# Kernel tuning notes

Measured on AMD Instinct MI355X. Metric: run time of the kernel, lower is better.

Reference implementation:

```python
import jax, jax.numpy as jnp
import numpy as np

B, C_IN, L = 16, 64, 1024
HID, OUT, ORDER = 1024, 512, 4
EPS = 1e-5


def setup_inputs() -> dict:
    key = jax.random.key(0)
    ks = jax.random.split(key, 4)
    return {
        "x": jax.random.normal(ks[0], (B, C_IN, L), jnp.float32),
        "W_in": jax.random.normal(ks[1], (C_IN, HID), jnp.float32) / np.sqrt(C_IN).astype(np.float32),
        "b_in": jnp.zeros((HID,), jnp.float32),
        "coeffs1": jax.random.normal(ks[2], (HID, HID, ORDER), jnp.float32) * 0.01,
        "bias1": jnp.zeros((HID,), jnp.float32),
        "g1": jnp.ones((HID,), jnp.float32),
        "beta1": jnp.zeros((HID,), jnp.float32),
        "coeffs2": jax.random.normal(ks[3], (OUT, HID, ORDER), jnp.float32) * 0.01,
        "bias2": jnp.zeros((OUT,), jnp.float32),
        "g2": jnp.ones((OUT,), jnp.float32),
        "beta2": jnp.zeros((OUT,), jnp.float32),
    }


def _taylor_kan(x, coeffs, bias):
    # x: (B, L, C_in); coeffs: (out, C_in, order); y[b,l,o] = sum_i sum_c x^i * coeffs[o,c,i]
    # Expressed as order-wise GEMMs with a running power -- no (B,out,L,C) expand.
    order = coeffs.shape[-1]
    y = jnp.zeros(x.shape[:2] + (coeffs.shape[0],), x.dtype)
    xp = jnp.ones_like(x)  # x**0 (matches torch 0**0 == 1)
    for i in range(order):
        y = y + jnp.einsum('blc,oc->blo', xp, coeffs[:, :, i])
        if i + 1 < order:
            xp = xp * x
    return y + bias


def _layernorm(x, g, b):
    mu = jnp.mean(x, -1, keepdims=True)
    var = jnp.mean((x - mu) ** 2, -1, keepdims=True)
    return (x - mu) * jax.lax.rsqrt(var + EPS) * g + b


def reference(x, W_in, b_in, coeffs1, bias1, g1, beta1, coeffs2, bias2, g2, beta2):
    # x: (B, C_in, L) -> project channels to hidden: (B, L, HID)
    h = jnp.einsum('bcl,ch->blh', x, W_in) + b_in
    h = _taylor_kan(h, coeffs1, bias1)            # (B, L, HID)
    h = jax.nn.gelu(_layernorm(h, g1, beta1), approximate=False)
    h = _taylor_kan(h, coeffs2, bias2)            # (B, L, OUT)
    h = _layernorm(h, g2, beta2)
    return jnp.mean(h, axis=1)                    # adaptive avg pool over L -> (B, OUT)
```

## Files before the change

### kernel.cpp

```cpp
#include <hip/hip_runtime.h>
#include <hip/hip_bf16.h>
#include <math.h>

#define Bsz  16
#define CIN  64
#define LEN  1024
#define HIDN 1024
#define OUTN 512
#define MTOT (Bsz*LEN)
#define KTOT (3*HIDN)
#define KT1  (2*HIDN + CIN)
#define LCHUNKS 32
#define LROWS   (LEN/LCHUNKS)

typedef __attribute__((ext_vector_type(8))) short bf16x8;
typedef __attribute__((ext_vector_type(16))) float f32x16;

__device__ __forceinline__ unsigned short f2bf(float x) {
    union { float f; unsigned int u; } v; v.f = x;
    unsigned int r = v.u + 0x7fff + ((v.u >> 16) & 1);
    return (unsigned short)(r >> 16);
}
__device__ __forceinline__ float bf2f(unsigned short u) {
    union { unsigned int u; float f; } v; v.u = ((unsigned int)u) << 16;
    return v.f;
}
__device__ __forceinline__ void gload_lds16(const void* g, void* l) {
    __builtin_amdgcn_global_load_lds((const __attribute__((address_space(1))) void*)g,
                                     (__attribute__((address_space(3))) void*)l, 16, 0, 0);
}
__device__ __forceinline__ void powfrags(const bf16x8& a, bf16x8& a2, bf16x8& a3) {
#pragma unroll
    for (int j = 0; j < 4; j++) {
        float f0 = bf2f((unsigned short)a[2 * j]);
        float f1 = bf2f((unsigned short)a[2 * j + 1]);
        float s0 = f0 * f0, s1 = f1 * f1;
        __hip_bfloat162 p2 = __float22bfloat162_rn(float2{ s0, s1 });
        __hip_bfloat162 p3 = __float22bfloat162_rn(float2{ s0 * f0, s1 * f1 });
        ((unsigned int*)&a2)[j] = *(unsigned int*)&p2;
        ((unsigned int*)&a3)[j] = *(unsigned int*)&p3;
    }
}

__global__ __launch_bounds__(256) void prep_all(const float* __restrict__ coeffs1,
                                                const float* __restrict__ bias1,
                                                const float* __restrict__ coeffs2,
                                                const float* __restrict__ bias2,
                                                const float* __restrict__ x,
                                                const float* __restrict__ Win,
                                                unsigned short* __restrict__ W1T,
                                                float* __restrict__ b1e,
                                                unsigned short* __restrict__ W2T,
                                                float* __restrict__ b2e,
                                                unsigned short* __restrict__ xT,
                                                unsigned short* __restrict__ WinT) {
    __shared__ float sm[64 * 65];
    int bid = blockIdx.x, t = threadIdx.x;
    if (bid < 1024) {
        int o = bid;
        float s = 0.f;
        unsigned short* wrow = W1T + (size_t)o * KT1;
        for (int c = t; c < HIDN; c += 256) {
            float4 v = *(const float4*)(coeffs1 + ((size_t)o * HIDN + c) * 4);
            s += v.x;
            wrow[c]        = f2bf(v.z);
            wrow[HIDN + c] = f2bf(v.w);
        }
        for (int off = 32; off > 0; off >>= 1) s += __shfl_down(s, off, 64);
        if ((t & 63) == 0) sm[t >> 6] = s;
        __syncthreads();
        if (t == 0) b1e[o] = bias1[o] + sm[0] + sm[1] + sm[2] + sm[3];
    } else if (bid < 1536) {
        int o = bid - 1024;
        float s = 0.f;
        unsigned short* wrow = W2T + (size_t)o * KTOT;
        for (int c = t; c < HIDN; c += 256) {
            float4 v = *(const float4*)(coeffs2 + ((size_t)o * HIDN + c) * 4);
            s += v.x;
            wrow[c]            = f2bf(v.y);
            wrow[HIDN + c]     = f2bf(v.z);
            wrow[2 * HIDN + c] = f2bf(v.w);
        }
        for (int off = 32; off > 0; off >>= 1) s += __shfl_down(s, off, 64);
        if ((t & 63) == 0) sm[t >> 6] = s;
        __syncthreads();
        if (t == 0) b2e[o] = bias2[o] + sm[0] + sm[1] + sm[2] + sm[3];
    } else {
        const float* src; unsigned short* dstbase; size_t src_rstride;
        int c0;
        if (bid < 1792) {
            int tile = bid - 1536; int b = tile >> 4; c0 = (tile & 15) * 64;
            src = x + (size_t)b * CIN * LEN;  src_rstride = LEN;
            dstbase = xT + ((size_t)b * LEN + c0) * CIN;
        } else {
            int tile = bid - 1792; c0 = tile * 64;
            src = Win; src_rstride = HIDN;
            dstbase = WinT + (size_t)c0 * CIN;
        }
#pragma unroll
        for (int it = 0; it < 4; it++) {
            int idx = t + it * 256;
            int c = idx >> 4, q = idx & 15;
            float4 v = *(const float4*)(src + (size_t)c * src_rstride + c0 + q * 4);
            sm[c * 65 + q * 4 + 0] = v.x;
            sm[c * 65 + q * 4 + 1] = v.y;
            sm[c * 65 + q * 4 + 2] = v.z;
            sm[c * 65 + q * 4 + 3] = v.w;
        }
        __syncthreads();
        int ll = t >> 2, cg = (t & 3) * 16;
        unsigned short* dst = dstbase + (size_t)ll * CIN + cg;
#pragma unroll
        for (int j = 0; j < 4; j++) {
            int c = cg + j * 4;
            ushort4 w = { f2bf(sm[(c + 0) * 65 + ll]), f2bf(sm[(c + 1) * 65 + ll]),
                          f2bf(sm[(c + 2) * 65 + ll]), f2bf(sm[(c + 3) * 65 + ll]) };
            *(ushort4*)(dst + j * 4) = w;
        }
    }
}

__global__ __launch_bounds__(256) void proj_mfma(const unsigned short* __restrict__ xT,
                                                 const unsigned short* __restrict__ WinT,
                                                 const float* __restrict__ bin,
                                                 unsigned short* __restrict__ A1,
                                                 const float* __restrict__ coeffs1,
                                                 unsigned short* __restrict__ W1T,
                                                 float* __restrict__ b1e) {
    __shared__ unsigned short smem[2 * 128 * 64];
    unsigned short* As = smem;
    unsigned short* Bs = smem + 128 * 64;
    unsigned short* ht = smem;
    int t = threadIdx.x, lane = t & 63, wave = t >> 6;
    int m0 = blockIdx.x * 128, n0 = blockIdx.y * 128;
    int srow = lane >> 3, sgcc = (lane & 7) ^ srow;
    const unsigned short* Ab = xT + (size_t)m0 * CIN;
    const unsigned short* Bb = WinT + (size_t)n0 * CIN;

    f32x16 acc[2][2] = {};
    int wr = (wave >> 1) * 64, wc = (wave & 1) * 64;
    int row32 = lane & 31, half = lane >> 5;

#pragma unroll
    for (int j = 0; j < 4; j++) {
        int rgrp = wave * 32 + j * 8;
        gload_lds16(Ab + (size_t)(rgrp + srow) * CIN + sgcc * 8, As + rgrp * 64);
        gload_lds16(Bb + (size_t)(rgrp + srow) * CIN + sgcc * 8, Bs + rgrp * 64);
    }
    __syncthreads();
#pragma unroll
    for (int ks = 0; ks < 4; ks++) {
        int cidx = ks * 2 + half;
        bf16x8 af[2], bf[2];
#pragma unroll
        for (int mt = 0; mt < 2; mt++) {
            int r = wr + mt * 32 + row32;
            af[mt] = *(const bf16x8*)(As + r * 64 + ((cidx ^ (r & 7)) << 3));
        }
#pragma unroll
        for (int nt = 0; nt < 2; nt++) {
            int c = wc + nt * 32 + row32;
            bf[nt] = *(const bf16x8*)(Bs + c * 64 + ((cidx ^ (c & 7)) << 3));
        }
#pragma unroll
        for (int mt = 0; mt < 2; mt++)
#pragma unroll
            for (int nt = 0; nt < 2; nt++)
                acc[mt][nt] = __builtin_amdgcn_mfma_f32_32x32x16_bf16(af[mt], bf[nt], acc[mt][nt], 0, 0, 0);
    }
    __syncthreads();
#pragma unroll
    for (int nt = 0; nt < 2; nt++) {
        int ocl = wc + nt * 32 + row32;
        float bo = bin[n0 + ocl];
#pragma unroll
        for (int mt = 0; mt < 2; mt++) {
#pragma unroll
            for (int reg = 0; reg < 16; reg++) {
                int rl = wr + mt * 32 + (reg & 3) + 8 * (reg >> 2) + 4 * half;
                ht[rl * 128 + ocl] = f2bf(acc[mt][nt][reg] + bo);
            }
        }
    }
    __syncthreads();
#pragma unroll
    for (int p = 0; p < 8; p++) {
        int r = p * 16 + (t >> 4);
        int c = (t & 15) * 8;
        bf16x8 hv = *(const bf16x8*)(ht + r * 128 + c);
        bf16x8 h2v, h3v;
#pragma unroll
        for (int j = 0; j < 8; j++) {
            float f = bf2f((unsigned short)hv[j]);
            float f2 = f * f;
            h2v[j] = (short)f2bf(f2);
            h3v[j] = (short)f2bf(f2 * f);
        }
        unsigned short* d = A1 + (size_t)(m0 + r) * KT1 + n0 + c;
        *(bf16x8*)(d)        = h2v;
        *(bf16x8*)(d + HIDN) = h3v;
    }
    if (n0 == 0) {
#pragma unroll
        for (int it = 0; it < 4; it++) {
            int idx = t + it * 256;
            int r = idx >> 3, cc = (idx & 7) * 8;
            bf16x8 v = *(const bf16x8*)(xT + (size_t)(m0 + r) * CIN + cc);
            *(bf16x8*)(A1 + (size_t)(m0 + r) * KT1 + 2 * HIDN + cc) = v;
        }
    }
    int o = blockIdx.x * 8 + blockIdx.y;
    __syncthreads();
    float* c1s   = (float*)smem;
    float* part  = (float*)smem + 1024;
    float* pbred = part + 256;
    for (int c = t; c < HIDN; c += 256) {
        float4 v = *(const float4*)(coeffs1 + ((size_t)o * HIDN + c) * 4);
        c1s[c] = v.y;
    }
    __syncthreads();
    float a1 = 0.f;
    int cbase = wave * 256;
    for (int c = cbase; c < cbase + 256; c++)
        a1 += bf2f(WinT[c * CIN + lane]) * c1s[c];
    part[wave * 64 + lane] = a1;
    float pb = 0.f;
    for (int c = t; c < HIDN; c += 256) pb += bin[c] * c1s[c];
    for (int off = 32; off > 0; off >>= 1) pb += __shfl_down(pb, off, 64);
    if (lane == 0) pbred[wave] = pb;
    __syncthreads();
    if (t < 64) {
        float v = part[t] + part[64 + t] + part[128 + t] + part[192 + t];
        W1T[(size_t)o * KT1 + 2 * HIDN + t] = f2bf(v);
    }
    if (t == 0) atomicAdd(&b1e[o], pbred[0] + pbred[1] + pbred[2] + pbred[3]);
}

template<int N, int KT, bool BF16OUT>
__global__ __launch_bounds__(256) void mfma_gemm(const unsigned short* __restrict__ A,
                                                 const unsigned short* __restrict__ BT,
                                                 const float* __restrict__ beff,
                                                 void* __restrict__ Yv) {
    __shared__ unsigned short As[128 * 64];
    __shared__ unsigned short Bs[128 * 64];
    int t = threadIdx.x;
    int lane = t & 63, wave = t >> 6;
    int m0 = blockIdx.x * 128, n0 = blockIdx.y * 128;
    const unsigned short* Ab = A + (size_t)m0 * KT;
    const unsigned short* Bb = BT + (size_t)n0 * KT;

    int srow = lane >> 3;
    int sgcc = (lane & 7) ^ srow;

    f32x16 acc[2][2] = {};
    int wr = (wave >> 1) * 64;
    int wc = (wave & 1) * 64;
    int row32 = lane & 31, half = lane >> 5;

    for (int k0 = 0; k0 < KT; k0 += 64) {
#pragma unroll
        for (int j = 0; j < 4; j++) {
            int rgrp = wave * 32 + j * 8;
            gload_lds16(Ab + ((size_t)(rgrp + srow) * KT + k0 + sgcc * 8), As + rgrp * 64);
            gload_lds16(Bb + ((size_t)(rgrp + srow) * KT + k0 + sgcc * 8), Bs + rgrp * 64);
        }
        __syncthreads();
#pragma unroll
        for (int ks = 0; ks < 4; ks++) {
            int cidx = ks * 2 + half;
            bf16x8 af[2], bf[2];
#pragma unroll
            for (int mt = 0; mt < 2; mt++) {
                int r = wr + mt * 32 + row32;
                af[mt] = *(const bf16x8*)(As + r * 64 + ((cidx ^ (r & 7)) << 3));
            }
#pragma unroll
            for (int nt = 0; nt < 2; nt++) {
                int c = wc + nt * 32 + row32;
                bf[nt] = *(const bf16x8*)(Bs + c * 64 + ((cidx ^ (c & 7)) << 3));
            }
#pragma unroll
            for (int mt = 0; mt < 2; mt++)
#pragma unroll
                for (int nt = 0; nt < 2; nt++)
                    acc[mt][nt] = __builtin_amdgcn_mfma_f32_32x32x16_bf16(af[mt], bf[nt], acc[mt][nt], 0, 0, 0);
        }
        __syncthreads();
    }
#pragma unroll
    for (int nt = 0; nt < 2; nt++) {
        int oc = n0 + wc + nt * 32 + row32;
        float bo = beff[oc];
#pragma unroll
        for (int mt = 0; mt < 2; mt++) {
#pragma unroll
            for (int reg = 0; reg < 16; reg++) {
                int rl = (reg & 3) + 8 * (reg >> 2) + 4 * half;
                int mr = m0 + wr + mt * 32 + rl;
                float v = acc[mt][nt][reg] + bo;
                if (BF16OUT) ((unsigned short*)Yv)[(size_t)mr * N + oc] = f2bf(v);
                else         ((float*)Yv)[(size_t)mr * N + oc] = v;
            }
        }
    }
}

__global__ __launch_bounds__(256) void ln_gelu(const unsigned short* __restrict__ y1,
                                               const float* __restrict__ g,
                                               const float* __restrict__ be,
                                               unsigned short* __restrict__ Gonly) {
    __shared__ float2 red[2][2];
    int t = threadIdx.x;
    int rhalf = t >> 7, l = t & 127, wid = (t >> 6) & 1;
    int m = blockIdx.x * 2 + rhalf;
    bf16x8 u = *(const bf16x8*)(y1 + (size_t)m * HIDN + l * 8);
    float v[8];
    float s = 0.f, ss = 0.f;
#pragma unroll
    for (int j = 0; j < 8; j++) {
        v[j] = bf2f((unsigned short)u[j]);
        s += v[j]; ss += v[j] * v[j];
    }
    for (int off = 32; off > 0; off >>= 1) {
        s  += __shfl_down(s, off, 64);
        ss += __shfl_down(ss, off, 64);
    }
    if ((t & 63) == 0) red[rhalf][wid] = make_float2(s, ss);
    __syncthreads();
    float sT  = red[rhalf][0].x + red[rhalf][1].x;
    float ssT = red[rhalf][0].y + red[rhalf][1].y;
    float mu = sT * (1.f / HIDN);
    float var = ssT * (1.f / HIDN) - mu * mu;
    float rs = rsqrtf(var + 1e-5f);
    float4 gA = *(const float4*)(g + l * 8),  gB = *(const float4*)(g + l * 8 + 4);
    float4 bA = *(const float4*)(be + l * 8), bB = *(const float4*)(be + l * 8 + 4);
    float gv[8] = { gA.x, gA.y, gA.z, gA.w, gB.x, gB.y, gB.z, gB.w };
    float bv[8] = { bA.x, bA.y, bA.z, bA.w, bB.x, bB.y, bB.z, bB.w };
    bf16x8 p1;
#pragma unroll
    for (int j = 0; j < 8; j++) {
        float xn = (v[j] - mu) * rs * gv[j] + bv[j];
        float gl = xn * 0.5f * (1.f + erff(xn * 0.70710678118654752f));
        p1[j] = (short)f2bf(gl);
    }
    *(bf16x8*)(Gonly + (size_t)m * HIDN + l * 8) = p1;
}

__global__ __launch_bounds__(256) void kan2_gemm(const unsigned short* __restrict__ G,
                                                 const unsigned short* __restrict__ W2T,
                                                 const float* __restrict__ beff,
                                                 unsigned short* __restrict__ Y) {
    __shared__ unsigned short smem[128 * 64 * 4];
    unsigned short* As = smem;
    unsigned short* Bs = smem + 128 * 64;
    int t = threadIdx.x, lane = t & 63, wave = t >> 6;
    int m0 = blockIdx.x * 128, n0 = blockIdx.y * 128;
    int srow = lane >> 3, sgcc = (lane & 7) ^ srow;
    const unsigned short* Ab = G + (size_t)m0 * HIDN;
    const unsigned short* Bb = W2T + (size_t)n0 * KTOT;

    f32x16 acc[2][2] = {};
    int wr = (wave >> 1) * 64, wc = (wave & 1) * 64;
    int row32 = lane & 31, half = lane >> 5;

    for (int c0 = 0; c0 < HIDN; c0 += 64) {
#pragma unroll
        for (int j = 0; j < 4; j++) {
            int rgrp = wave * 32 + j * 8;
            gload_lds16(Ab + ((size_t)(rgrp + srow) * HIDN + c0 + sgcc * 8), As + rgrp * 64);
#pragma unroll
            for (int p = 0; p < 3; p++)
                gload_lds16(Bb + ((size_t)(rgrp + srow) * KTOT + p * HIDN + c0 + sgcc * 8),
                            Bs + p * 128 * 64 + rgrp * 64);
        }
        __syncthreads();
#pragma unroll
        for (int ks = 0; ks < 4; ks++) {
            int cidx = ks * 2 + half;
            bf16x8 af[2], af2[2], af3[2];
#pragma unroll
            for (int mt = 0; mt < 2; mt++) {
                int r = wr + mt * 32 + row32;
                af[mt] = *(const bf16x8*)(As + r * 64 + ((cidx ^ (r & 7)) << 3));
                powfrags(af[mt], af2[mt], af3[mt]);
            }
#pragma unroll
            for (int nt = 0; nt < 2; nt++) {
                int c = wc + nt * 32 + row32;
                int boff = c * 64 + ((cidx ^ (c & 7)) << 3);
                bf16x8 b1 = *(const bf16x8*)(Bs + boff);
                bf16x8 b2 = *(const bf16x8*)(Bs + 128 * 64 + boff);
                bf16x8 b3 = *(const bf16x8*)(Bs + 2 * 128 * 64 + boff);
#pragma unroll
                for (int mt = 0; mt < 2; mt++) {
                    acc[mt][nt] = __builtin_amdgcn_mfma_f32_32x32x16_bf16(af[mt],  b1, acc[mt][nt], 0, 0, 0);
                    acc[mt][nt] = __builtin_amdgcn_mfma_f32_32x32x16_bf16(af2[mt], b2, acc[mt][nt], 0, 0, 0);
                    acc[mt][nt] = __builtin_amdgcn_mfma_f32_32x32x16_bf16(af3[mt], b3, acc[mt][nt], 0, 0, 0);
                }
            }
        }
        __syncthreads();
    }
#pragma unroll
    for (int nt = 0; nt < 2; nt++) {
        int oc = n0 + wc + nt * 32 + row32;
        float bo = beff[oc];
#pragma unroll
        for (int mt = 0; mt < 2; mt++) {
#pragma unroll
            for (int reg = 0; reg < 16; reg++) {
                int rl = (reg & 3) + 8 * (reg >> 2) + 4 * half;
                int mr = m0 + wr + mt * 32 + rl;
                Y[(size_t)mr * OUTN + oc] = f2bf(acc[mt][nt][reg] + bo);
            }
        }
    }
}

__global__ __launch_bounds__(256) void ln_pool_partial(const unsigned short* __restrict__ y2,
                                                       const float* __restrict__ g,
                                                       const float* __restrict__ be,
                                                       float* __restrict__ partial) {
    __shared__ float part[4][OUTN];
    int t = threadIdx.x, lane = t & 63, wave = t >> 6;
    int b = blockIdx.x, chunk = blockIdx.y;
    int mbase = b * LEN + chunk * LROWS;

    float4 gA = *(const float4*)(g + 8 * lane),  gB = *(const float4*)(g + 8 * lane + 4);
    float4 bA = *(const float4*)(be + 8 * lane), bB = *(const float4*)(be + 8 * lane + 4);
    float gv[8] = { gA.x, gA.y, gA.z, gA.w, gB.x, gB.y, gB.z, gB.w };
    float bv[8] = { bA.x, bA.y, bA.z, bA.w, bB.x, bB.y, bB.z, bB.w };

    float acc[8] = {0.f, 0.f, 0.f, 0.f, 0.f, 0.f, 0.f, 0.f};
    for (int rr = wave; rr < LROWS; rr += 4) {
        bf16x8 u = *(const bf16x8*)(y2 + (size_t)(mbase + rr) * OUTN + 8 * lane);
        float v[8];
        float s = 0.f, ss = 0.f;
#pragma unroll
        for (int j = 0; j < 8; j++) {
            v[j] = bf2f((unsigned short)u[j]);
            s += v[j]; ss += v[j] * v[j];
        }
        for (int off = 32; off > 0; off >>= 1) {
            s  += __shfl_down(s, off, 64);
            ss += __shfl_down(ss, off, 64);
        }
        s  = __shfl(s, 0, 64);
        ss = __shfl(ss, 0, 64);
        float mu = s * (1.f / OUTN);
        float var = ss * (1.f / OUTN) - mu * mu;
        float rs = rsqrtf(var + 1e-5f);
#pragma unroll
        for (int j = 0; j < 8; j++)
            acc[j] += (v[j] - mu) * rs * gv[j] + bv[j];
    }
    *(float4*)(&part[wave][8 * lane])     = *(float4*)(&acc[0]);
    *(float4*)(&part[wave][8 * lane + 4]) = *(float4*)(&acc[4]);
    __syncthreads();
    float p0 = part[0][2*t] + part[1][2*t] + part[2][2*t] + part[3][2*t];
    float p1 = part[0][2*t+1] + part[1][2*t+1] + part[2][2*t+1] + part[3][2*t+1];
    float* dst = partial + ((size_t)b * LCHUNKS + chunk) * OUTN;
    *(float2*)(dst + 2 * t) = make_float2(p0, p1);
}

__global__ __launch_bounds__(256) void pool_reduce(const float* __restrict__ partial,
                                                   float* __restrict__ out) {
    int b = blockIdx.x, t = threadIdx.x;
    const float* src = partial + (size_t)b * LCHUNKS * OUTN;
    float s0 = 0.f, s1 = 0.f;
    for (int c = 0; c < LCHUNKS; c++) {
        float2 v = *(const float2*)(src + (size_t)c * OUTN + 2 * t);
        s0 += v.x; s1 += v.y;
    }
    *(float2*)(out + (size_t)b * OUTN + 2 * t) = make_float2(s0 * (1.f / LEN), s1 * (1.f / LEN));
}

extern "C" void kernel_launch(void* const* d_in, const int* in_sizes, int n_in,
                              void* d_out, int out_size, void* d_ws, size_t ws_size,
                              hipStream_t stream) {
    const float* x       = (const float*)d_in[0];
    const float* Win     = (const float*)d_in[1];
    const float* bin     = (const float*)d_in[2];
    const float* coeffs1 = (const float*)d_in[3];
    const float* bias1   = (const float*)d_in[4];
    const float* g1      = (const float*)d_in[5];
    const float* beta1   = (const float*)d_in[6];
    const float* coeffs2 = (const float*)d_in[7];
    const float* bias2   = (const float*)d_in[8];
    const float* g2      = (const float*)d_in[9];
    const float* beta2   = (const float*)d_in[10];
    float* out = (float*)d_out;

    char* ws = (char*)d_ws;
    unsigned short* A1    = (unsigned short*)ws;
    unsigned short* Gonly = (unsigned short*)ws;
    char* p1 = ws + (size_t)MTOT * KTOT * 2;
    unsigned short* y1   = (unsigned short*)p1;
    unsigned short* y2   = (unsigned short*)p1;
    char* p2 = p1 + (size_t)MTOT * HIDN * 2;
    unsigned short* W1T  = (unsigned short*)p2;
    char* p3 = p2 + (size_t)HIDN * KT1 * 2;
    unsigned short* W2T  = (unsigned short*)p3;
    char* p4 = p3 + (size_t)OUTN * KTOT * 2;
    float* b1e = (float*)p4;
    float* b2e = (float*)(p4 + HIDN * sizeof(float));
    char* p5 = p4 + (HIDN + OUTN) * sizeof(float);
    unsigned short* xT   = (unsigned short*)p5;
    char* p6 = p5 + (size_t)MTOT * CIN * 2;
    unsigned short* WinT = (unsigned short*)p6;
    float* partial = (float*)W1T;

    prep_all<<<1808, 256, 0, stream>>>(coeffs1, bias1, coeffs2, bias2, x, Win,
                                       W1T, b1e, W2T, b2e, xT, WinT);
    proj_mfma<<<dim3(MTOT / 128, HIDN / 128), 256, 0, stream>>>(xT, WinT, bin, A1,
                                                                coeffs1, W1T, b1e);
    mfma_gemm<HIDN, KT1, true><<<dim3(MTOT / 128, HIDN / 128), 256, 0, stream>>>(A1, W1T, b1e, y1);
    ln_gelu<<<MTOT / 2, 256, 0, stream>>>(y1, g1, beta1, Gonly);
    kan2_gemm<<<dim3(MTOT / 128, OUTN / 128), 256, 0, stream>>>(Gonly, W2T, b2e, y2);
    ln_pool_partial<<<dim3(Bsz, LCHUNKS), 256, 0, stream>>>(y2, g2, beta2, partial);
    pool_reduce<<<Bsz, 256, 0, stream>>>(partial, out);
}
```

Baseline: 286.9 us.

## Compute h² and h³ inside the first KAN GEMM instead of materializing them

```diff
diff --git a/kernel.cpp b/kernel.cpp
--- a/kernel.cpp
+++ b/kernel.cpp
@@ -9,7 +9,7 @@
 #define OUTN 512
 #define MTOT (Bsz*LEN)
 #define KTOT (3*HIDN)
-#define KT1  (2*HIDN + CIN)
+#define KT1H (2*HIDN)
 #define LCHUNKS 32
 #define LROWS   (LEN/LCHUNKS)
 
@@ -59,7 +59,7 @@
     if (bid < 1024) {
         int o = bid;
         float s = 0.f;
-        unsigned short* wrow = W1T + (size_t)o * KT1;
+        unsigned short* wrow = W1T + (size_t)o * KT1H;
         for (int c = t; c < HIDN; c += 256) {
             float4 v = *(const float4*)(coeffs1 + ((size_t)o * HIDN + c) * 4);
             s += v.x;
@@ -120,13 +120,39 @@
     }
 }
 
+__global__ __launch_bounds__(256) void wc1_kernel(const float* __restrict__ coeffs1,
+                                                  const unsigned short* __restrict__ WinT,
+                                                  const float* __restrict__ bin,
+                                                  unsigned short* __restrict__ WC1,
+                                                  float* __restrict__ b1e) {
+    __shared__ float c1s[HIDN];
+    __shared__ float part[4][64];
+    __shared__ float pbred[4];
+    int o = blockIdx.x, t = threadIdx.x, lane = t & 63, wave = t >> 6;
+    for (int c = t; c < HIDN; c += 256)
+        c1s[c] = coeffs1[((size_t)o * HIDN + c) * 4 + 1];
+    __syncthreads();
+    float acc = 0.f;
+    int cbase = wave * 256;
+    for (int c = cbase; c < cbase + 256; c++)
+        acc += bf2f(WinT[c * CIN + lane]) * c1s[c];
+    part[wave][lane] = acc;
+    float pb = 0.f;
+    for (int c = t; c < HIDN; c += 256) pb += bin[c] * c1s[c];
+    for (int off = 32; off > 0; off >>= 1) pb += __shfl_down(pb, off, 64);
+    if (lane == 0) pbred[wave] = pb;
+    __syncthreads();
+    if (t < 64) {
+        float v = part[0][t] + part[1][t] + part[2][t] + part[3][t];
+        WC1[(size_t)o * CIN + t] = f2bf(v);
+    }
+    if (t == 0) b1e[o] += pbred[0] + pbred[1] + pbred[2] + pbred[3];
+}
+
 __global__ __launch_bounds__(256) void proj_mfma(const unsigned short* __restrict__ xT,
                                                  const unsigned short* __restrict__ WinT,
                                                  const float* __restrict__ bin,
-                                                 unsigned short* __restrict__ A1,
-                                                 const float* __restrict__ coeffs1,
-                                                 unsigned short* __restrict__ W1T,
-                                                 float* __restrict__ b1e) {
+                                                 unsigned short* __restrict__ Hout) {
     __shared__ unsigned short smem[2 * 128 * 64];
     unsigned short* As = smem;
     unsigned short* Bs = smem + 128 * 64;
@@ -188,104 +214,91 @@
         int r = p * 16 + (t >> 4);
         int c = (t & 15) * 8;
         bf16x8 hv = *(const bf16x8*)(ht + r * 128 + c);
-        bf16x8 h2v, h3v;
-#pragma unroll
-        for (int j = 0; j < 8; j++) {
-            float f = bf2f((unsigned short)hv[j]);
-            float f2 = f * f;
-            h2v[j] = (short)f2bf(f2);
-            h3v[j] = (short)f2bf(f2 * f);
-        }
-        unsigned short* d = A1 + (size_t)(m0 + r) * KT1 + n0 + c;
-        *(bf16x8*)(d)        = h2v;
-        *(bf16x8*)(d + HIDN) = h3v;
-    }
-    if (n0 == 0) {
-#pragma unroll
-        for (int it = 0; it < 4; it++) {
-            int idx = t + it * 256;
-            int r = idx >> 3, cc = (idx & 7) * 8;
-            bf16x8 v = *(const bf16x8*)(xT + (size_t)(m0 + r) * CIN + cc);
-            *(bf16x8*)(A1 + (size_t)(m0 + r) * KT1 + 2 * HIDN + cc) = v;
-        }
-    }
-    int o = blockIdx.x * 8 + blockIdx.y;
-    __syncthreads();
-    float* c1s   = (float*)smem;
-    float* part  = (float*)smem + 1024;
-    float* pbred = part + 256;
-    for (int c = t; c < HIDN; c += 256) {
-        float4 v = *(const float4*)(coeffs1 + ((size_t)o * HIDN + c) * 4);
-        c1s[c] = v.y;
-    }
-    __syncthreads();
-    float a1 = 0.f;
-    int cbase = wave * 256;
-    for (int c = cbase; c < cbase + 256; c++)
-        a1 += bf2f(WinT[c * CIN + lane]) * c1s[c];
-    part[wave * 64 + lane] = a1;
-    float pb = 0.f;
-    for (int c = t; c < HIDN; c += 256) pb += bin[c] * c1s[c];
-    for (int off = 32; off > 0; off >>= 1) pb += __shfl_down(pb, off, 64);
-    if (lane == 0) pbred[wave] = pb;
-    __syncthreads();
-    if (t < 64) {
-        float v = part[t] + part[64 + t] + part[128 + t] + part[192 + t];
-        W1T[(size_t)o * KT1 + 2 * HIDN + t] = f2bf(v);
-    }
-    if (t == 0) atomicAdd(&b1e[o], pbred[0] + pbred[1] + pbred[2] + pbred[3]);
-}
-
-template<int N, int KT, bool BF16OUT>
-__global__ __launch_bounds__(256) void mfma_gemm(const unsigned short* __restrict__ A,
-                                                 const unsigned short* __restrict__ BT,
+        *(bf16x8*)(Hout + (size_t)(m0 + r) * HIDN + n0 + c) = hv;
+    }
+}
+
+__global__ __launch_bounds__(256) void kan1_gemm(const unsigned short* __restrict__ H,
+                                                 const unsigned short* __restrict__ xT,
+                                                 const unsigned short* __restrict__ W1T,
+                                                 const unsigned short* __restrict__ WC1,
                                                  const float* __restrict__ beff,
-                                                 void* __restrict__ Yv) {
-    __shared__ unsigned short As[128 * 64];
-    __shared__ unsigned short Bs[128 * 64];
-    int t = threadIdx.x;
-    int lane = t & 63, wave = t >> 6;
+                                                 unsigned short* __restrict__ Y) {
+    __shared__ unsigned short smem[128 * 64 * 3];
+    unsigned short* As = smem;
+    unsigned short* Bs = smem + 128 * 64;
+    int t = threadIdx.x, lane = t & 63, wave = t >> 6;
     int m0 = blockIdx.x * 128, n0 = blockIdx.y * 128;
-    const unsigned short* Ab = A + (size_t)m0 * KT;
-    const unsigned short* Bb = BT + (size_t)n0 * KT;
-
-    int srow = lane >> 3;
-    int sgcc = (lane & 7) ^ srow;
+    int srow = lane >> 3, sgcc = (lane & 7) ^ srow;
+    const unsigned short* Ab = H + (size_t)m0 * HIDN;
+    const unsigned short* Bb = W1T + (size_t)n0 * KT1H;
 
     f32x16 acc[2][2] = {};
-    int wr = (wave >> 1) * 64;
-    int wc = (wave & 1) * 64;
+    int wr = (wave >> 1) * 64, wc = (wave & 1) * 64;
     int row32 = lane & 31, half = lane >> 5;
 
-    for (int k0 = 0; k0 < KT; k0 += 64) {
+    for (int c0 = 0; c0 < HIDN; c0 += 64) {
 #pragma unroll
         for (int j = 0; j < 4; j++) {
             int rgrp = wave * 32 + j * 8;
-            gload_lds16(Ab + ((size_t)(rgrp + srow) * KT + k0 + sgcc * 8), As + rgrp * 64);
-            gload_lds16(Bb + ((size_t)(rgrp + srow) * KT + k0 + sgcc * 8), Bs + rgrp * 64);
+            gload_lds16(Ab + ((size_t)(rgrp + srow) * HIDN + c0 + sgcc * 8), As + rgrp * 64);
+#pragma unroll
+            for (int p = 0; p < 2; p++)
+                gload_lds16(Bb + ((size_t)(rgrp + srow) * KT1H + p * HIDN + c0 + sgcc * 8),
+                            Bs + p * 128 * 64 + rgrp * 64);
         }
         __syncthreads();
 #pragma unroll
         for (int ks = 0; ks < 4; ks++) {
             int cidx = ks * 2 + half;
-            bf16x8 af[2], bf[2];
+            bf16x8 af2[2], af3[2];
 #pragma unroll
             for (int mt = 0; mt < 2; mt++) {
                 int r = wr + mt * 32 + row32;
-                af[mt] = *(const bf16x8*)(As + r * 64 + ((cidx ^ (r & 7)) << 3));
+                bf16x8 af = *(const bf16x8*)(As + r * 64 + ((cidx ^ (r & 7)) << 3));
+                powfrags(af, af2[mt], af3[mt]);
             }
 #pragma unroll
             for (int nt = 0; nt < 2; nt++) {
                 int c = wc + nt * 32 + row32;
-                bf[nt] = *(const bf16x8*)(Bs + c * 64 + ((cidx ^ (c & 7)) << 3));
-            }
-#pragma unroll
-            for (int mt = 0; mt < 2; mt++)
-#pragma unroll
-                for (int nt = 0; nt < 2; nt++)
-                    acc[mt][nt] = __builtin_amdgcn_mfma_f32_32x32x16_bf16(af[mt], bf[nt], acc[mt][nt], 0, 0, 0);
-        }
-        __syncthreads();
+                int boff = c * 64 + ((cidx ^ (c & 7)) << 3);
+                bf16x8 b2 = *(const bf16x8*)(Bs + boff);
+                bf16x8 b3 = *(const bf16x8*)(Bs + 128 * 64 + boff);
+#pragma unroll
+                for (int mt = 0; mt < 2; mt++) {
+                    acc[mt][nt] = __builtin_amdgcn_mfma_f32_32x32x16_bf16(af2[mt], b2, acc[mt][nt], 0, 0, 0);
+                    acc[mt][nt] = __builtin_amdgcn_mfma_f32_32x32x16_bf16(af3[mt], b3, acc[mt][nt], 0, 0, 0);
+                }
+            }
+        }
+        __syncthreads();
+    }
+#pragma unroll
+    for (int j = 0; j < 4; j++) {
+        int rgrp = wave * 32 + j * 8;
+        gload_lds16(xT  + (size_t)(m0 + rgrp + srow) * CIN + sgcc * 8, As + rgrp * 64);
+        gload_lds16(WC1 + (size_t)(n0 + rgrp + srow) * CIN + sgcc * 8, Bs + rgrp * 64);
+    }
+    __syncthreads();
+#pragma unroll
+    for (int ks = 0; ks < 4; ks++) {
+        int cidx = ks * 2 + half;
+        bf16x8 af[2], bf[2];
+#pragma unroll
+        for (int mt = 0; mt < 2; mt++) {
+            int r = wr + mt * 32 + row32;
+            af[mt] = *(const bf16x8*)(As + r * 64 + ((cidx ^ (r & 7)) << 3));
+        }
+#pragma unroll
+        for (int nt = 0; nt < 2; nt++) {
+            int c = wc + nt * 32 + row32;
+            bf[nt] = *(const bf16x8*)(Bs + c * 64 + ((cidx ^ (c & 7)) << 3));
+        }
+#pragma unroll
+        for (int mt = 0; mt < 2; mt++)
+#pragma unroll
+            for (int nt = 0; nt < 2; nt++)
+                acc[mt][nt] = __builtin_amdgcn_mfma_f32_32x32x16_bf16(af[mt], bf[nt], acc[mt][nt], 0, 0, 0);
     }
 #pragma unroll
     for (int nt = 0; nt < 2; nt++) {
@@ -297,9 +310,7 @@
             for (int reg = 0; reg < 16; reg++) {
                 int rl = (reg & 3) + 8 * (reg >> 2) + 4 * half;
                 int mr = m0 + wr + mt * 32 + rl;
-                float v = acc[mt][nt][reg] + bo;
-                if (BF16OUT) ((unsigned short*)Yv)[(size_t)mr * N + oc] = f2bf(v);
-                else         ((float*)Yv)[(size_t)mr * N + oc] = v;
+                Y[(size_t)mr * HIDN + oc] = f2bf(acc[mt][nt][reg] + bo);
             }
         }
     }
@@ -492,14 +503,14 @@
     float* out = (float*)d_out;
 
     char* ws = (char*)d_ws;
-    unsigned short* A1    = (unsigned short*)ws;
+    unsigned short* Hpln  = (unsigned short*)ws;
     unsigned short* Gonly = (unsigned short*)ws;
-    char* p1 = ws + (size_t)MTOT * KTOT * 2;
+    char* p1 = ws + (size_t)MTOT * HIDN * 2;
     unsigned short* y1   = (unsigned short*)p1;
     unsigned short* y2   = (unsigned short*)p1;
     char* p2 = p1 + (size_t)MTOT * HIDN * 2;
     unsigned short* W1T  = (unsigned short*)p2;
-    char* p3 = p2 + (size_t)HIDN * KT1 * 2;
+    char* p3 = p2 + (size_t)HIDN * KT1H * 2;
     unsigned short* W2T  = (unsigned short*)p3;
     char* p4 = p3 + (size_t)OUTN * KTOT * 2;
     float* b1e = (float*)p4;
@@ -508,13 +519,15 @@
     unsigned short* xT   = (unsigned short*)p5;
     char* p6 = p5 + (size_t)MTOT * CIN * 2;
     unsigned short* WinT = (unsigned short*)p6;
+    char* p7 = p6 + (size_t)HIDN * CIN * 2;
+    unsigned short* WC1  = (unsigned short*)p7;
     float* partial = (float*)W1T;
 
     prep_all<<<1808, 256, 0, stream>>>(coeffs1, bias1, coeffs2, bias2, x, Win,
                                        W1T, b1e, W2T, b2e, xT, WinT);
-    proj_mfma<<<dim3(MTOT / 128, HIDN / 128), 256, 0, stream>>>(xT, WinT, bin, A1,
-                                                                coeffs1, W1T, b1e);
-    mfma_gemm<HIDN, KT1, true><<<dim3(MTOT / 128, HIDN / 128), 256, 0, stream>>>(A1, W1T, b1e, y1);
+    wc1_kernel<<<HIDN, 256, 0, stream>>>(coeffs1, WinT, bin, WC1, b1e);
+    proj_mfma<<<dim3(MTOT / 128, HIDN / 128), 256, 0, stream>>>(xT, WinT, bin, Hpln);
+    kan1_gemm<<<dim3(MTOT / 128, HIDN / 128), 256, 0, stream>>>(Hpln, xT, W1T, WC1, b1e, y1);
     ln_gelu<<<MTOT / 2, 256, 0, stream>>>(y1, g1, beta1, Gonly);
     kan2_gemm<<<dim3(MTOT / 128, OUTN / 128), 256, 0, stream>>>(Gonly, W2T, b2e, y2);
     ln_pool_partial<<<dim3(Bsz, LCHUNKS), 256, 0, stream>>>(y2, g2, beta2, partial);
```

New measurement: 290.7 us (median of 2 runs). Within noise of the previous version (+1.3%).
